# Performance work log

Hardware: AMD Instinct MI355X
Metric: run time of the kernel (lower is better)

## Reference

```python
import jax, jax.numpy as jnp
import numpy as np
from jax import lax

SAMPLE_RATE = 44100
MAX_DELAY_MS = 1000.0
MAX_DELAY_SAMPLES = int(MAX_DELAY_MS * SAMPLE_RATE / 1000)  # 44100
DELAY_MS = 500.0
FEEDBACK = 0.3
MIX = 0.5
DELAY_SAMPLES = min(int(DELAY_MS * SAMPLE_RATE / 1000), MAX_DELAY_SAMPLES)  # 22050

B, T = 64, 441000  # T is a multiple of DELAY_SAMPLES (20 blocks)


def setup_inputs() -> dict:
    key = jax.random.key(0)
    x = jax.random.normal(key, (B, T), dtype=jnp.float32)
    return {"x": x}


def _delay_feedback(x):
    # Circular buffer with buffer_size > max_delay_samples is equivalent to a
    # fixed lag-D linear recurrence:
    #   delayed[t] = 0                         , t <  D
    #   delayed[t] = x[t-D] + fb*delayed[t-D]  , t >= D
    #   out[t]     = x[t]*(1-mix) + delayed[t]*mix
    # Within a block of D consecutive samples, delayed depends only on the
    # previous block -> scan over T//D blocks, each block fully vectorized.
    D = DELAY_SAMPLES
    b, t = x.shape
    n_blk = t // D
    xb = x.reshape(b, n_blk, D).transpose(1, 0, 2)  # (n_blk, B, D)

    def step(carry, xk):
        # carry = buffer contents written one block (D samples) ago
        delayed = carry
        out = xk * (1.0 - MIX) + delayed * MIX
        new_carry = xk + FEEDBACK * delayed
        return new_carry, out

    init = jnp.zeros((b, D), dtype=x.dtype)
    _, outs = lax.scan(step, init, xb)  # outs: (n_blk, B, D)
    return outs.transpose(1, 0, 2).reshape(b, t)


def reference(x) -> jnp.ndarray:
    return _delay_feedback(x)
```

## Files before the change

kernel.cpp:

```cpp
#include <hip/hip_runtime.h>


constexpr int   kB    = 64;
constexpr int   kT    = 441000;
constexpr int   kD    = 22050;
constexpr int   kNBLK = kT / kD;
constexpr float kFB   = 0.3f;
constexpr float kMIX  = 0.5f;

constexpr int kHALF  = kD / 2;
constexpr int kTOTAL = kB * kHALF;

__global__ __launch_bounds__(256)
void delay_scan_kernel(const float* __restrict__ x, float* __restrict__ out) {
    int tid = blockIdx.x * blockDim.x + threadIdx.x;
    if (tid >= kTOTAL) return;
    int b = tid / kHALF;
    int i = tid - b * kHALF;

    const float2* __restrict__ xp =
        reinterpret_cast<const float2*>(x + (size_t)b * kT) + i;
    float2* __restrict__ op =
        reinterpret_cast<float2*>(out + (size_t)b * kT) + i;

    constexpr int kSTRIDE2 = kD / 2;

    float2 xv[kNBLK];
    #pragma unroll
    for (int k = 0; k < kNBLK; ++k)
        xv[k] = xp[(size_t)k * kSTRIDE2];

    float2 carry; carry.x = 0.0f; carry.y = 0.0f;
    #pragma unroll
    for (int k = 0; k < kNBLK; ++k) {
        float2 o;
        o.x = xv[k].x * (1.0f - kMIX) + carry.x * kMIX;
        o.y = xv[k].y * (1.0f - kMIX) + carry.y * kMIX;
        op[(size_t)k * kSTRIDE2] = o;

        carry.x = xv[k].x + kFB * carry.x;
        carry.y = xv[k].y + kFB * carry.y;
    }
}

extern "C" void kernel_launch(void* const* d_in, const int* in_sizes, int n_in,
                              void* d_out, int out_size, void* d_ws, size_t ws_size,
                              hipStream_t stream) {
    const float* x = (const float*)d_in[0];
    float* out = (float*)d_out;

    constexpr int kBlock = 256;
    constexpr int kGrid  = (kTOTAL + kBlock - 1) / kBlock;
    delay_scan_kernel<<<kGrid, kBlock, 0, stream>>>(x, out);
}
```

Before: 199.3 us.

## Process two columns per thread with nontemporal loads/stores and rolling prefetch

Each thread now handles two adjacent float2 columns, halving the thread count. All loads and stores use nontemporal builtins to bypass cache retention, and the up-front load of all 20 blocks is replaced by a one-step-ahead prefetch. This targets cache pollution and register pressure, but it lowers the number of loads in flight per thread and the total thread count, which can hurt latency hiding.

```diff
diff --git a/kernel.cpp b/kernel.cpp
--- a/kernel.cpp
+++ b/kernel.cpp
@@ -1,5 +1,7 @@
 #include <hip/hip_runtime.h>
 
+
+typedef float f2 __attribute__((ext_vector_type(2)));
 
 constexpr int   kB    = 64;
 constexpr int   kT    = 441000;
@@ -9,37 +11,52 @@
 constexpr float kMIX  = 0.5f;
 
 constexpr int kHALF  = kD / 2;
-constexpr int kTOTAL = kB * kHALF;
+constexpr int kCOLS  = kB * kHALF;
+constexpr int kPAIRS = kCOLS / 2;
 
 __global__ __launch_bounds__(256)
 void delay_scan_kernel(const float* __restrict__ x, float* __restrict__ out) {
-    int tid = blockIdx.x * blockDim.x + threadIdx.x;
-    if (tid >= kTOTAL) return;
-    int b = tid / kHALF;
-    int i = tid - b * kHALF;
+    int t = blockIdx.x * blockDim.x + threadIdx.x;
+    if (t >= kPAIRS) return;
 
-    const float2* __restrict__ xp =
-        reinterpret_cast<const float2*>(x + (size_t)b * kT) + i;
-    float2* __restrict__ op =
-        reinterpret_cast<float2*>(out + (size_t)b * kT) + i;
+    int c0 = 2 * t;
+    int c1 = c0 + 1;
+    int b0 = c0 / kHALF, i0 = c0 - b0 * kHALF;
+    int b1 = c1 / kHALF, i1 = c1 - b1 * kHALF;
 
-    constexpr int kSTRIDE2 = kD / 2;
+    const f2* __restrict__ xa = reinterpret_cast<const f2*>(x + (size_t)b0 * kT) + i0;
+    const f2* __restrict__ xb = reinterpret_cast<const f2*>(x + (size_t)b1 * kT) + i1;
+    f2* __restrict__ oa = reinterpret_cast<f2*>(out + (size_t)b0 * kT) + i0;
+    f2* __restrict__ ob = reinterpret_cast<f2*>(out + (size_t)b1 * kT) + i1;
 
-    float2 xv[kNBLK];
-    #pragma unroll
-    for (int k = 0; k < kNBLK; ++k)
-        xv[k] = xp[(size_t)k * kSTRIDE2];
+    constexpr int kS = kD / 2;
 
-    float2 carry; carry.x = 0.0f; carry.y = 0.0f;
+    f2 ca; ca.x = 0.0f; ca.y = 0.0f;
+    f2 cb; cb.x = 0.0f; cb.y = 0.0f;
+
+    f2 va = __builtin_nontemporal_load(xa);
+    f2 vb = __builtin_nontemporal_load(xb);
+
     #pragma unroll
     for (int k = 0; k < kNBLK; ++k) {
-        float2 o;
-        o.x = xv[k].x * (1.0f - kMIX) + carry.x * kMIX;
-        o.y = xv[k].y * (1.0f - kMIX) + carry.y * kMIX;
-        op[(size_t)k * kSTRIDE2] = o;
+        f2 na, nb;
+        if (k + 1 < kNBLK) {
+            na = __builtin_nontemporal_load(xa + (size_t)(k + 1) * kS);
+            nb = __builtin_nontemporal_load(xb + (size_t)(k + 1) * kS);
+        }
 
-        carry.x = xv[k].x + kFB * carry.x;
-        carry.y = xv[k].y + kFB * carry.y;
+        f2 o0, o1;
+        o0.x = va.x * (1.0f - kMIX) + ca.x * kMIX;
+        o0.y = va.y * (1.0f - kMIX) + ca.y * kMIX;
+        o1.x = vb.x * (1.0f - kMIX) + cb.x * kMIX;
+        o1.y = vb.y * (1.0f - kMIX) + cb.y * kMIX;
+        __builtin_nontemporal_store(o0, oa + (size_t)k * kS);
+        __builtin_nontemporal_store(o1, ob + (size_t)k * kS);
+
+        ca.x = va.x + kFB * ca.x;  ca.y = va.y + kFB * ca.y;
+        cb.x = vb.x + kFB * cb.x;  cb.y = vb.y + kFB * cb.y;
+
+        va = na; vb = nb;
     }
 }
 
@@ -50,6 +67,6 @@
     float* out = (float*)d_out;
 
     constexpr int kBlock = 256;
-    constexpr int kGrid  = (kTOTAL + kBlock - 1) / kBlock;
+    constexpr int kGrid  = (kPAIRS + kBlock - 1) / kBlock;
     delay_scan_kernel<<<kGrid, kBlock, 0, stream>>>(x, out);
 }
```

New measurement: 213.1 us. 1.07x slower.
